# Kernel optimization log

Hardware: AMD Instinct MI355X
Metric: run time of the kernel (lower is better)

## Reference

```python
import jax, jax.numpy as jnp
from jax import lax
import numpy as np

KSIZE = 3        # matching kernel size
RATE = 2         # downsample rate; raw kernel = 2*RATE = 4
FUSE_K = 3       # fusion (diagonal-sum) kernel size
SOFTMAX_SCALE = 10.0
EPS = 1e-4


def extract_patches(x, k, s, pad):
    """im2col: x [B,C,H,W] -> patches [B, L, C, k, k], L = oH*oW (row-major),
    matching torch.nn.Unfold ordering after the view/permute in the source."""
    B, C, H, W = x.shape
    xp = jnp.pad(x, ((0, 0), (0, 0), (pad, pad), (pad, pad)))
    Hp, Wp = H + 2 * pad, W + 2 * pad
    oH = (Hp - k) // s + 1
    oW = (Wp - k) // s + 1
    cols = []
    for i in range(k):
        for j in range(k):
            cols.append(xp[:, :, i:i + (oH - 1) * s + 1:s, j:j + (oW - 1) * s + 1:s])
    p = jnp.stack(cols, axis=0).reshape(k, k, B, C, oH, oW)
    return p.transpose(2, 4, 5, 3, 0, 1).reshape(B, oH * oW, C, k, k)


def fuse_diag(y, k):
    """conv2d with identity (eye(k)) kernel, 'same' padding == sum of diagonal shifts."""
    r = k // 2
    n0, n1 = y.shape
    yp = jnp.pad(y, r)
    return sum(yp[r + d:r + d + n0, r + d:r + d + n1] for d in range(-r, r + 1))


def _per_sample(xi, wi, raw_wi, mi):
    # xi: [C,Hs,Ws] downsampled foreground; wi: [L,C,3,3] bg patches;
    # raw_wi: [L,C,4,4] raw bg patches; mi: [L] patch validity mask
    C, Hs, Ws = xi.shape
    L = wi.shape[0]
    # L2-normalize each background patch (EPS added per-element inside the sum, as in source)
    wi_norm = jnp.sqrt(jnp.sum(wi * wi + EPS, axis=(1, 2, 3), keepdims=True))
    wn = (wi / wi_norm).reshape(L, -1)                      # [L, C*9]
    # correlation scores: conv2d(xi, wi_normed, pad=1) expressed as a GEMM over im2col patches
    fp = extract_patches(xi[None], KSIZE, 1, KSIZE // 2)[0].reshape(L, -1)  # [L_f, C*9]
    yi = wn @ fp.T                                          # [L_b, L_f]
    # fusion trick: identity-kernel conv along both diagonal orientations
    yi = fuse_diag(yi, FUSE_K)
    yi = yi.reshape(Hs, Ws, Hs, Ws).transpose(1, 0, 3, 2).reshape(L, L)
    yi = fuse_diag(yi, FUSE_K)
    yi = yi.reshape(Ws, Hs, Ws, Hs).transpose(1, 0, 3, 2)
    yi = yi.reshape(L, Hs, Ws)
    m = mi[:, None, None]
    yi = jax.nn.softmax(yi * m * SOFTMAX_SCALE, axis=0) * m  # softmax over bg-patch axis
    # transposed conv reconstruction with raw 4x4 patches, stride=RATE, padding=1
    k = 2 * RATE
    w_t = jnp.flip(raw_wi, (2, 3)).transpose(1, 0, 2, 3)     # [C, L, 4, 4] OIHW
    out = lax.conv_general_dilated(
        yi[None], w_t, window_strides=(1, 1),
        padding=[(k - 1 - 1, k - 1 - 1)] * 2, lhs_dilation=(RATE, RATE),
        dimension_numbers=('NCHW', 'OIHW', 'NCHW'))[0] / 4.0  # [C, H, W]
    return out


def setup_inputs() -> dict:
    key = jax.random.key(0)
    k1, k2 = jax.random.split(key)
    B, C, H, W = 4, 128, 96, 96
    b = jax.random.normal(k1, (B, C, H, W), jnp.float32)
    f = jax.random.normal(k2, (B, C, H, W), jnp.float32)
    mask = jnp.ones((B, 1, H, W), jnp.float32)
    return {"b": b, "f": f, "mask": mask}


def reference(b, f, mask):
    B, C, H, W = b.shape
    k_raw = 2 * RATE
    # raw patches from full-res background: k=4, stride=2, pad=1 (get_pad 'valid')
    raw_w = extract_patches(b, k_raw, RATE, 1)               # [B, L, C, 4, 4]
    # nearest downsample by RATE (F.interpolate nearest, scale 1/rate)
    fs = f[:, :, ::RATE, ::RATE]
    bs = b[:, :, ::RATE, ::RATE]
    Hs, Ws = fs.shape[2], fs.shape[3]
    w = extract_patches(bs, KSIZE, 1, KSIZE // 2)            # [B, L, C, 3, 3]
    ms = mask.shape[3] // Ws
    m_small = mask[:, :, ::ms, ::ms]                         # [B, 1, Hs, Ws]
    m = extract_patches(m_small, KSIZE, 1, KSIZE // 2)       # [B, L, 1, 3, 3]
    mm = (jnp.mean(m, axis=(2, 3, 4)) == 1.0).astype(jnp.float32)  # [B, L]
    y = jax.vmap(_per_sample)(fs, w, raw_w, mm)              # [B, C, H, W]
    return y
```

## Files before the change

kernel.cpp:

```cpp
#include <hip/hip_runtime.h>
#include <hip/hip_bf16.h>
#include <math.h>

#define NS   4
#define CH   128
#define HW   96
#define GS   48
#define LL   2304
#define CKN  2048
#define SCALE 10.0f
#define EPSSUM 0.1152f
#define PCH2 32
#define NCH2 72

#define S_IN  ((size_t)CH * HW * HW)
#define S_MK  ((size_t)HW * HW)
#define S_BS  ((size_t)CH * LL)
#define S_PM  ((size_t)NCH2 * LL)
#define S_BUF ((size_t)LL * LL)
#define S_W2  ((size_t)CKN * LL)
#define S_AT  ((size_t)LL * LL)

typedef __attribute__((ext_vector_type(8))) short short8;
typedef __attribute__((ext_vector_type(4))) float float4v;

#define GLDS16(gptr, lptr) \
    __builtin_amdgcn_global_load_lds((const __attribute__((address_space(1))) void*)(gptr), \
        (__attribute__((address_space(3))) void*)(lptr), 16, 0, 0)

__device__ __forceinline__ float4 ld4(const float* p) { return *reinterpret_cast<const float4*>(p); }


__global__ __launch_bounds__(256) void k_stage(const float* __restrict__ b, const float* __restrict__ f,
                                               float* __restrict__ bs_c, float* __restrict__ fs_c) {
    int s = blockIdx.z;
    b += s * S_IN; f += s * S_IN; bs_c += s * S_BS; fs_c += s * S_BS;
    int c  = blockIdx.y;
    int rs = blockIdx.x * 256 + threadIdx.x;
    int r = rs / GS, ss = rs % GS;
    int src = c * HW * HW + (2 * r) * HW + 2 * ss;
    bs_c[c * LL + rs] = b[src];
    fs_c[c * LL + rs] = f[src];
}

__global__ __launch_bounds__(256) void k_ssq(const float* __restrict__ bs_c, float* __restrict__ ssq) {
    int s = blockIdx.z;
    bs_c += s * S_BS; ssq += (size_t)s * LL;
    int rs = blockIdx.x * 256 + threadIdx.x;
    int c0 = blockIdx.y * 32;
    float acc = 0.f;
    for (int c = c0; c < c0 + 32; ++c) { float v = bs_c[c * LL + rs]; acc += v * v; }
    atomicAdd(&ssq[rs], acc);
}

__global__ __launch_bounds__(256) void k_norm_mm(const float* __restrict__ ssq, const float* __restrict__ mk,
                                                 float* __restrict__ invn, float* __restrict__ mmv) {
    int sI = blockIdx.z;
    ssq += (size_t)sI * LL; mk += sI * S_MK; invn += (size_t)sI * LL; mmv += (size_t)sI * LL;
    int p = blockIdx.x * 256 + threadIdx.x;
    int ph = p / GS, pw = p % GS;
    float acc = EPSSUM;
    float msum = 0.f;
    for (int di = -1; di <= 1; ++di)
        for (int dj = -1; dj <= 1; ++dj) {
            int r = ph + di, s = pw + dj;
            if (r >= 0 && r < GS && s >= 0 && s < GS) {
                acc  += ssq[r * GS + s];
                msum += mk[(2 * r) * HW + 2 * s];
            }
        }
    invn[p] = 1.0f / sqrtf(acc);
    mmv[p]  = (msum / 9.0f == 1.0f) ? 1.0f : 0.0f;
}

__global__ __launch_bounds__(256) void k_w2T(const float* __restrict__ b, __hip_bfloat16* __restrict__ W2T) {
    int sI = blockIdx.z;
    b += sI * S_IN; W2T += sI * S_W2;
    int ck = blockIdx.y;
    int p  = blockIdx.x * 256 + threadIdx.x;
    int c = ck >> 4, dy = (ck >> 2) & 3, dx = ck & 3;
    int ph = p / GS, pw = p % GS;
    int r = 2 * ph + dy - 1, s = 2 * pw + dx - 1;
    float v = 0.f;
    if (r >= 0 && r < HW && s >= 0 && s < HW) v = b[c * HW * HW + r * HW + s];
    W2T[(size_t)ck * LL + p] = __float2bfloat16(v);
}

__global__ __launch_bounds__(256) void k_split_T(const float* __restrict__ bs_c, const float* __restrict__ fs_c,
                                                 float* __restrict__ bufB) {
    __shared__ float tile[32][33];
    int z = blockIdx.z;
    int s = z >> 1, sel = z & 1;
    const float* X = (sel ? fs_c : bs_c) + s * S_BS;
    __hip_bfloat16* base = (__hip_bfloat16*)(bufB + s * S_BUF);
    __hip_bfloat16* hi = base + (size_t)sel * 2 * LL * CH;
    __hip_bfloat16* lo = hi + (size_t)LL * CH;
    int r0 = blockIdx.x * 32, c0 = blockIdx.y * 32;
    int tx = threadIdx.x & 31, ty = threadIdx.x >> 5;
#pragma unroll
    for (int j = 0; j < 4; ++j)
        tile[ty + 8 * j][tx] = X[(size_t)(c0 + ty + 8 * j) * LL + r0 + tx];
    __syncthreads();
#pragma unroll
    for (int j = 0; j < 4; ++j) {
        int rl = ty + 8 * j, cl = tx;
        float v = tile[cl][rl];
        __hip_bfloat16 h = __float2bfloat16(v);
        float resid = v - __bfloat162float(h);
        hi[(size_t)(r0 + rl) * CH + c0 + cl] = h;
        lo[(size_t)(r0 + rl) * CH + c0 + cl] = __float2bfloat16(resid);
    }
}

__global__ __launch_bounds__(256) void gemm1_mfma(const float* __restrict__ bufB, float* __restrict__ bufA) {
    __shared__ __hip_bfloat16 sAh[128 * 32];
    __shared__ __hip_bfloat16 sAl[128 * 32];
    __shared__ __hip_bfloat16 sBh[128 * 32];
    __shared__ __hip_bfloat16 sBl[128 * 32];
    int sI = blockIdx.z;
    const __hip_bfloat16* base = (const __hip_bfloat16*)(bufB + sI * S_BUF);
    const __hip_bfloat16* Ahi = base;
    const __hip_bfloat16* Alo = Ahi + (size_t)LL * CH;
    const __hip_bfloat16* Bhi = Alo + (size_t)LL * CH;
    const __hip_bfloat16* Blo = Bhi + (size_t)LL * CH;
    float* C = bufA + sI * S_BUF;

    int t = threadIdx.x, lane = t & 63, w = t >> 6;
    int wr = w >> 1, wc = w & 1;
    int m0 = blockIdx.y * 128, n0 = blockIdx.x * 128;

    float4v acc[4][4];
#pragma unroll
    for (int i = 0; i < 4; ++i)
#pragma unroll
        for (int j = 0; j < 4; ++j) acc[i][j] = (float4v){0.f, 0.f, 0.f, 0.f};

    for (int k0 = 0; k0 < 128; k0 += 32) {
#pragma unroll
        for (int it = 0; it < 2; ++it) {
            int chunk = it * 256 + w * 64 + lane;
            int row = chunk >> 2, ps = chunk & 3;
            int pd = ps ^ (row & 3);
            size_t ga = (size_t)(m0 + row) * 128 + k0 + pd * 8;
            size_t gb = (size_t)(n0 + row) * 128 + k0 + pd * 8;
            GLDS16(Ahi + ga, (char*)sAh + (size_t)chunk * 16);
            GLDS16(Alo + ga, (char*)sAl + (size_t)chunk * 16);
            GLDS16(Bhi + gb, (char*)sBh + (size_t)chunk * 16);
            GLDS16(Blo + gb, (char*)sBl + (size_t)chunk * 16);
        }
        __syncthreads();

        int lrow = lane & 15, part = lane >> 4;
        int sw = part ^ (lrow & 3);
        short8 ah[4], al[4], bh[4], bl[4];
#pragma unroll
        for (int i = 0; i < 4; ++i) {
            int slot = (wr * 64 + i * 16 + lrow) * 4 + sw;
            ah[i] = *reinterpret_cast<const short8*>(sAh + (size_t)slot * 8);
            al[i] = *reinterpret_cast<const short8*>(sAl + (size_t)slot * 8);
        }
#pragma unroll
        for (int j = 0; j < 4; ++j) {
            int slot = (wc * 64 + j * 16 + lrow) * 4 + sw;
            bh[j] = *reinterpret_cast<const short8*>(sBh + (size_t)slot * 8);
            bl[j] = *reinterpret_cast<const short8*>(sBl + (size_t)slot * 8);
        }
#pragma unroll
        for (int i = 0; i < 4; ++i)
#pragma unroll
            for (int j = 0; j < 4; ++j) {
                acc[i][j] = __builtin_amdgcn_mfma_f32_16x16x32_bf16(ah[i], bh[j], acc[i][j], 0, 0, 0);
                acc[i][j] = __builtin_amdgcn_mfma_f32_16x16x32_bf16(ah[i], bl[j], acc[i][j], 0, 0, 0);
                acc[i][j] = __builtin_amdgcn_mfma_f32_16x16x32_bf16(al[i], bh[j], acc[i][j], 0, 0, 0);
            }
        __syncthreads();
    }

    int col = lane & 15, rbase = (lane >> 4) * 4;
#pragma unroll
    for (int i = 0; i < 4; ++i)
#pragma unroll
        for (int j = 0; j < 4; ++j)
#pragma unroll
            for (int r = 0; r < 4; ++r) {
                int m = m0 + wr * 64 + i * 16 + rbase + r;
                int n = n0 + wc * 64 + j * 16 + col;
                C[(size_t)m * LL + n] = acc[i][j][r];
            }
}

__global__ __launch_bounds__(256) void gemm2_mfma(const __hip_bfloat16* __restrict__ W2T_,
                                                  const __hip_bfloat16* __restrict__ attnT_,
                                                  float* __restrict__ bufB) {
    __shared__ __hip_bfloat16 As[128 * 32];
    __shared__ __hip_bfloat16 Bs[128 * 32];
    int sI = blockIdx.z;
    const __hip_bfloat16* A = W2T_ + sI * S_W2;
    const __hip_bfloat16* B = attnT_ + sI * S_AT;
    __hip_bfloat16* C = (__hip_bfloat16*)(bufB + sI * S_BUF);

    int t = threadIdx.x;
    int lane = t & 63, w = t >> 6;
    int wr = w >> 1, wc = w & 1;
    int m0 = blockIdx.y * 128, n0 = blockIdx.x * 128;

    float4v acc[4][4];
#pragma unroll
    for (int i = 0; i < 4; ++i)
#pragma unroll
        for (int j = 0; j < 4; ++j) acc[i][j] = (float4v){0.f, 0.f, 0.f, 0.f};

    for (int k0 = 0; k0 < LL; k0 += 32) {
#pragma unroll
        for (int it = 0; it < 2; ++it) {
            int chunk = it * 256 + w * 64 + lane;
            int row = chunk >> 2, ps = chunk & 3;
            int pd = ps ^ (row & 3);
            const __hip_bfloat16* ga = A + (size_t)(m0 + row) * LL + k0 + pd * 8;
            const __hip_bfloat16* gb = B + (size_t)(n0 + row) * LL + k0 + pd * 8;
            GLDS16(ga, (char*)As + (size_t)chunk * 16);
            GLDS16(gb, (char*)Bs + (size_t)chunk * 16);
        }
        __syncthreads();

        int lrow = lane & 15, part = lane >> 4;
        int sw = part ^ (lrow & 3);
        short8 afrag[4], bfrag[4];
#pragma unroll
        for (int i = 0; i < 4; ++i) {
            int slot = (wr * 64 + i * 16 + lrow) * 4 + sw;
            afrag[i] = *reinterpret_cast<const short8*>(As + (size_t)slot * 8);
        }
#pragma unroll
        for (int j = 0; j < 4; ++j) {
            int slot = (wc * 64 + j * 16 + lrow) * 4 + sw;
            bfrag[j] = *reinterpret_cast<const short8*>(Bs + (size_t)slot * 8);
        }
#pragma unroll
        for (int i = 0; i < 4; ++i)
#pragma unroll
            for (int j = 0; j < 4; ++j)
                acc[i][j] = __builtin_amdgcn_mfma_f32_16x16x32_bf16(afrag[i], bfrag[j], acc[i][j], 0, 0, 0);
        __syncthreads();
    }

    int col = lane & 15, rbase = (lane >> 4) * 4;
#pragma unroll
    for (int i = 0; i < 4; ++i)
#pragma unroll
        for (int j = 0; j < 4; ++j)
#pragma unroll
            for (int r = 0; r < 4; ++r) {
                int m = m0 + wr * 64 + i * 16 + rbase + r;
                int n = n0 + wc * 64 + j * 16 + col;
                C[(size_t)m * LL + n] = __float2bfloat16(acc[i][j][r]);
            }
}

__global__ __launch_bounds__(192) void k_corr_v4(const float* __restrict__ bufA, const float* __restrict__ invn,
                                                 float* __restrict__ bufB) {
    int sI = blockIdx.z;
    const float* D = bufA + sI * S_BUF;
    float* yi = bufB + sI * S_BUF;
    invn += (size_t)sI * LL;

    int p  = blockIdx.y;
    int qi = blockIdx.x * 192 + threadIdx.x;
    int q4 = qi * 4;
    int qh = q4 / GS, qw0 = q4 % GS;
    int ph = p / GS, pw = p % GS;

    float4 acc = {0.f, 0.f, 0.f, 0.f};
#pragma unroll
    for (int di = -1; di <= 1; ++di) {
        int rp = ph + di, tq = qh + di;
        if (rp < 0 || rp >= GS || tq < 0 || tq >= GS) continue;
        int r0 = rp * GS + pw;
        int c0 = tq * GS + qw0;
        {
            float4 Cc = ld4(D + (size_t)r0 * LL + c0);
            acc.x += Cc.x; acc.y += Cc.y; acc.z += Cc.z; acc.w += Cc.w;
        }
        if (pw > 0) {
            const float* rowm = D + (size_t)(r0 - 1) * LL;
            float4 L  = ld4(rowm + (qw0 > 0 ? c0 - 4 : c0));
            float4 Cm = ld4(rowm + c0);
            acc.x += (qw0 > 0 ? L.w : 0.f);
            acc.y += Cm.x; acc.z += Cm.y; acc.w += Cm.z;
        }
        if (pw < GS - 1) {
            const float* rowp = D + (size_t)(r0 + 1) * LL;
            float4 Cp = ld4(rowp + c0);
            float4 R  = ld4(rowp + (qw0 < GS - 4 ? c0 + 4 : c0));
            acc.x += Cp.y; acc.y += Cp.z; acc.z += Cp.w;
            acc.w += (qw0 < GS - 4 ? R.x : 0.f);
        }
    }
    float inv = invn[p];
    float4 outv = {inv * acc.x, inv * acc.y, inv * acc.z, inv * acc.w};
    *reinterpret_cast<float4*>(yi + (size_t)p * LL + q4) = outv;
}

__device__ __forceinline__ int gmap(int x) { int hi = x / GS; int lo = x - hi * GS; return lo * GS + hi; }

__global__ __launch_bounds__(256) void k_fuse2_sm(const float* __restrict__ bufB, const float* __restrict__ mmv,
                                                  float* __restrict__ bufA,
                                                  float* __restrict__ pmax, float* __restrict__ psum) {
    int sI = blockIdx.z;
    const float* yi = bufB + sI * S_BUF;
    float* S2 = bufA + sI * S_BUF;
    mmv += (size_t)sI * LL; pmax += sI * S_PM; psum += sI * S_PM;
    int q = blockIdx.x * 256 + threadIdx.x;
    int qh = q / GS, qw = q % GS;
    int b0 = qw * GS + qh;
    int p0 = blockIdx.y * PCH2;
    float mx = -1e30f, sm = 0.f;
    for (int i = 0; i < PCH2; ++i) {
        int p = p0 + i;
        int ph = p / GS, pw = p % GS;
        int a0 = pw * GS + ph;
        float s = 0.f;
#pragma unroll
        for (int e = -1; e <= 1; ++e) {
            int ae = a0 + e, be = b0 + e;
            if (ae < 0 || ae >= LL || be < 0 || be >= LL) continue;
            int A = gmap(ae), B = gmap(be);
#pragma unroll
            for (int d = -1; d <= 1; ++d) {
                int Ad = A + d, Bd = B + d;
                if (Ad >= 0 && Ad < LL && Bd >= 0 && Bd < LL)
                    s += yi[(size_t)Ad * LL + Bd];
            }
        }
        S2[(size_t)p * LL + q] = s;
        float lg = (mmv[p] != 0.f) ? SCALE * s : 0.f;
        float nm = fmaxf(mx, lg);
        sm = sm * __expf(mx - nm) + __expf(lg - nm);
        mx = nm;
    }
    pmax[blockIdx.y * LL + q] = mx;
    psum[blockIdx.y * LL + q] = sm;
}

__global__ __launch_bounds__(256) void k_sm2(const float* __restrict__ pmax, const float* __restrict__ psum,
                                             float* __restrict__ Mq, float* __restrict__ Dq) {
    __shared__ float red[4][64];
    int sI = blockIdx.z;
    pmax += sI * S_PM; psum += sI * S_PM; Mq += (size_t)sI * LL; Dq += (size_t)sI * LL;
    int t = threadIdx.x;
    int ql = t & 63, g = t >> 6;
    int q = blockIdx.x * 64 + ql;
    float mx = -1e30f;
    for (int ch = g * 18; ch < g * 18 + 18; ++ch) mx = fmaxf(mx, pmax[(size_t)ch * LL + q]);
    red[g][ql] = mx;
    __syncthreads();
    float mall = fmaxf(fmaxf(red[0][ql], red[1][ql]), fmaxf(red[2][ql], red[3][ql]));
    float sm = 0.f;
    for (int ch = g * 18; ch < g * 18 + 18; ++ch)
        sm += psum[(size_t)ch * LL + q] * __expf(pmax[(size_t)ch * LL + q] - mall);
    __syncthreads();
    red[g][ql] = sm;
    __syncthreads();
    if (g == 0) {
        Mq[q] = mall;
        Dq[q] = (red[0][ql] + red[1][ql]) + (red[2][ql] + red[3][ql]);
    }
}

__global__ __launch_bounds__(256) void k_sm3T(const float* __restrict__ S2buf, const float* __restrict__ mmv,
                                              const float* __restrict__ Mq, const float* __restrict__ Dq,
                                              __hip_bfloat16* __restrict__ attnT) {
    __shared__ float tile[32][33];
    int sI = blockIdx.z;
    const float* S2 = S2buf + sI * S_BUF;
    mmv += (size_t)sI * LL; Mq += (size_t)sI * LL; Dq += (size_t)sI * LL; attnT += sI * S_AT;
    int tx = threadIdx.x & 31, ty = threadIdx.x >> 5;
    int p0 = blockIdx.y * 32, q0 = blockIdx.x * 32;
    int q = q0 + tx;
    float mq = Mq[q], dq = Dq[q];
#pragma unroll
    for (int j = 0; j < 4; ++j) {
        int p = p0 + ty + 8 * j;
        float v = S2[(size_t)p * LL + q];
        float attn = (mmv[p] != 0.f) ? __expf(SCALE * v - mq) / dq : 0.f;
        tile[ty + 8 * j][tx] = attn;
    }
    __syncthreads();
#pragma unroll
    for (int j = 0; j < 4; ++j) {
        int qq = q0 + ty + 8 * j;
        attnT[(size_t)qq * LL + p0 + tx] = __float2bfloat16(tile[tx][ty + 8 * j]);
    }
}

__global__ __launch_bounds__(256) void k_out(const float* __restrict__ bufB, float* __restrict__ out) {
    int sI = blockIdx.z;
    const __hip_bfloat16* Z = (const __hip_bfloat16*)(bufB + sI * S_BUF);
    out += sI * S_IN;
    int c  = blockIdx.y;
    int yx = blockIdx.x * 256 + threadIdx.x;
    int y = yx / HW, x = yx % HW;
    int u = y >> 1, a = y & 1, v = x >> 1, w = x & 1;
    int qh1 = u + a - 1, qh2 = u + a, qw1 = v + w - 1, qw2 = v + w;
    int cb = c * 16;
    float s = 0.f;
    if (qh1 >= 0) {
        if (qw1 >= 0)  s += __bfloat162float(Z[(size_t)(cb + (3 - a) * 4 + (3 - w)) * LL + qh1 * GS + qw1]);
        if (qw2 < GS)  s += __bfloat162float(Z[(size_t)(cb + (3 - a) * 4 + (1 - w)) * LL + qh1 * GS + qw2]);
    }
    if (qh2 < GS) {
        if (qw1 >= 0)  s += __bfloat162float(Z[(size_t)(cb + (1 - a) * 4 + (3 - w)) * LL + qh2 * GS + qw1]);
        if (qw2 < GS)  s += __bfloat162float(Z[(size_t)(cb + (1 - a) * 4 + (1 - w)) * LL + qh2 * GS + qw2]);
    }
    out[(size_t)c * HW * HW + yx] = 0.25f * s;
}


extern "C" void kernel_launch(void* const* d_in, const int* in_sizes, int n_in,
                              void* d_out, int out_size, void* d_ws, size_t ws_size,
                              hipStream_t stream) {
    const float* b_all = (const float*)d_in[0];
    const float* f_all = (const float*)d_in[1];
    const float* m_all = (const float*)d_in[2];
    float* out = (float*)d_out;
    float* ws  = (float*)d_ws;

    const size_t perF = 2 * S_BS + 5 * (size_t)LL + 2 * S_PM + 2 * S_BUF + S_W2 / 2 + S_AT / 2;
    const size_t perB = perF * sizeof(float);
    int nb = (ws_size >= NS * perB) ? NS : ((ws_size >= 2 * perB) ? 2 : 1);

    size_t off = 0;
    float* bs_c = ws + off; off += nb * S_BS;
    float* fs_c = ws + off; off += nb * S_BS;
    float* ssq  = ws + off; off += nb * (size_t)LL;
    float* invn = ws + off; off += nb * (size_t)LL;
    float* mmv  = ws + off; off += nb * (size_t)LL;
    float* Mq   = ws + off; off += nb * (size_t)LL;
    float* Dq   = ws + off; off += nb * (size_t)LL;
    float* pmax = ws + off; off += nb * S_PM;
    float* psum = ws + off; off += nb * S_PM;
    float* bufA = ws + off; off += nb * S_BUF;
    float* bufB = ws + off; off += nb * S_BUF;
    __hip_bfloat16* W2T   = (__hip_bfloat16*)(ws + off); off += nb * S_W2 / 2;
    __hip_bfloat16* attnT = (__hip_bfloat16*)(ws + off); off += nb * S_AT / 2;

    for (int s0 = 0; s0 < NS; s0 += nb) {
        const float* b  = b_all + s0 * S_IN;
        const float* f  = f_all + s0 * S_IN;
        const float* mk = m_all + s0 * S_MK;
        float* outp = out + s0 * S_IN;

        hipMemsetAsync(ssq, 0, nb * LL * sizeof(float), stream);
        k_stage    <<<dim3(9, CH, nb), 256, 0, stream>>>(b, f, bs_c, fs_c);
        k_ssq      <<<dim3(9, 4, nb), 256, 0, stream>>>(bs_c, ssq);
        k_norm_mm  <<<dim3(9, 1, nb), 256, 0, stream>>>(ssq, mk, invn, mmv);
        k_w2T      <<<dim3(9, CKN, nb), 256, 0, stream>>>(b, W2T);
        k_split_T  <<<dim3(72, 4, 2 * nb), 256, 0, stream>>>(bs_c, fs_c, bufB);

        gemm1_mfma <<<dim3(18, 18, nb), 256, 0, stream>>>(bufB, bufA);
        k_corr_v4  <<<dim3(3, LL, nb), 192, 0, stream>>>(bufA, invn, bufB);
        k_fuse2_sm <<<dim3(9, NCH2, nb), 256, 0, stream>>>(bufB, mmv, bufA, pmax, psum);

        k_sm2      <<<dim3(36, 1, nb), 256, 0, stream>>>(pmax, psum, Mq, Dq);
        k_sm3T     <<<dim3(72, 72, nb), 256, 0, stream>>>(bufA, mmv, Mq, Dq, attnT);

        gemm2_mfma <<<dim3(LL / 128, CKN / 128, nb), 256, 0, stream>>>(W2T, attnT, bufB);
        k_out      <<<dim3(36, CH, nb), 256, 0, stream>>>(bufB, outp);
    }
}
```

Baseline: 587.4 us.

## Split diagonal fusion into separable passes with LDS ring buffer and vectorized second pass

Restructures the two diagonal-sum fusion stages. The first kernel now computes the normalized correlation rows and applies the first diagonal fusion in a rolling three-row shared-memory buffer, so each row is produced once. The second kernel reads the already-fused rows with float4 loads, producing four outputs per thread with per-column online softmax statistics, replacing the nine scattered loads per element. Buffer roles for gemm2 and the output kernel are swapped to fit the new dataflow. In exchange, the first kernel uses large blocks with shared memory and serialized barriers per row, and the second pass falls back to gathered loads at the boundaries.

```diff
diff --git a/kernel.cpp b/kernel.cpp
--- a/kernel.cpp
+++ b/kernel.cpp
@@ -12,6 +12,7 @@
 #define EPSSUM 0.1152f
 #define PCH2 32
 #define NCH2 72
+#define TPF  16
 
 #define S_IN  ((size_t)CH * HW * HW)
 #define S_MK  ((size_t)HW * HW)
@@ -191,13 +192,13 @@
 
 __global__ __launch_bounds__(256) void gemm2_mfma(const __hip_bfloat16* __restrict__ W2T_,
                                                   const __hip_bfloat16* __restrict__ attnT_,
-                                                  float* __restrict__ bufB) {
+                                                  float* __restrict__ bufA) {
     __shared__ __hip_bfloat16 As[128 * 32];
     __shared__ __hip_bfloat16 Bs[128 * 32];
     int sI = blockIdx.z;
     const __hip_bfloat16* A = W2T_ + sI * S_W2;
     const __hip_bfloat16* B = attnT_ + sI * S_AT;
-    __hip_bfloat16* C = (__hip_bfloat16*)(bufB + sI * S_BUF);
+    __hip_bfloat16* C = (__hip_bfloat16*)(bufA + sI * S_BUF);
 
     int t = threadIdx.x;
     int lane = t & 63, w = t >> 6;
@@ -257,89 +258,136 @@
             }
 }
 
-__global__ __launch_bounds__(192) void k_corr_v4(const float* __restrict__ bufA, const float* __restrict__ invn,
-                                                 float* __restrict__ bufB) {
+__global__ __launch_bounds__(576) void k_corr_fuse1(const float* __restrict__ bufA, const float* __restrict__ invn,
+                                                    float* __restrict__ bufB) {
+    __shared__ float L[3][LL];
     int sI = blockIdx.z;
     const float* D = bufA + sI * S_BUF;
-    float* yi = bufB + sI * S_BUF;
+    float* S1 = bufB + sI * S_BUF;
     invn += (size_t)sI * LL;
-
-    int p  = blockIdx.y;
+    int a0 = blockIdx.x * TPF;
+    int t = threadIdx.x;
+    int q4 = t * 4;
+    int qh = q4 / GS, qw0 = q4 % GS;
+
+    auto produce = [&](int p) {
+        int slot = ((p % 3) + 3) % 3;
+        float4 o = {0.f, 0.f, 0.f, 0.f};
+        if (p >= 0 && p < LL) {
+            int ph = p / GS, pw = p % GS;
+            float4 acc = {0.f, 0.f, 0.f, 0.f};
+#pragma unroll
+            for (int di = -1; di <= 1; ++di) {
+                int rp = ph + di, tq = qh + di;
+                if (rp < 0 || rp >= GS || tq < 0 || tq >= GS) continue;
+                int r0 = rp * GS + pw;
+                int c0 = tq * GS + qw0;
+                {
+                    float4 Cc = ld4(D + (size_t)r0 * LL + c0);
+                    acc.x += Cc.x; acc.y += Cc.y; acc.z += Cc.z; acc.w += Cc.w;
+                }
+                if (pw > 0) {
+                    const float* rowm = D + (size_t)(r0 - 1) * LL;
+                    float4 Lq = ld4(rowm + (qw0 > 0 ? c0 - 4 : c0));
+                    float4 Cm = ld4(rowm + c0);
+                    acc.x += (qw0 > 0 ? Lq.w : 0.f);
+                    acc.y += Cm.x; acc.z += Cm.y; acc.w += Cm.z;
+                }
+                if (pw < GS - 1) {
+                    const float* rowp = D + (size_t)(r0 + 1) * LL;
+                    float4 Cp = ld4(rowp + c0);
+                    float4 Rq = ld4(rowp + (qw0 < GS - 4 ? c0 + 4 : c0));
+                    acc.x += Cp.y; acc.y += Cp.z; acc.z += Cp.w;
+                    acc.w += (qw0 < GS - 4 ? Rq.x : 0.f);
+                }
+            }
+            float inv = invn[p];
+            o.x = inv * acc.x; o.y = inv * acc.y; o.z = inv * acc.z; o.w = inv * acc.w;
+        }
+        *reinterpret_cast<float4*>(&L[slot][q4]) = o;
+    };
+
+    produce(a0 - 1);
+    produce(a0);
+    __syncthreads();
+    for (int r = a0; r < a0 + TPF; ++r) {
+        produce(r + 1);
+        __syncthreads();
+        int sm1 = ((r - 1) % 3 + 3) % 3, s0 = r % 3, sp1 = (r + 1) % 3;
+        float4 acc = *reinterpret_cast<const float4*>(&L[s0][q4]);
+        {
+            float4 Cm = *reinterpret_cast<const float4*>(&L[sm1][q4]);
+            float lm = (q4 > 0) ? L[sm1][q4 - 1] : 0.f;
+            acc.x += lm; acc.y += Cm.x; acc.z += Cm.y; acc.w += Cm.z;
+        }
+        {
+            float4 Cp = *reinterpret_cast<const float4*>(&L[sp1][q4]);
+            float rp = (q4 + 4 < LL) ? L[sp1][q4 + 4] : 0.f;
+            acc.x += Cp.y; acc.y += Cp.z; acc.z += Cp.w; acc.w += rp;
+        }
+        *reinterpret_cast<float4*>(S1 + (size_t)r * LL + q4) = acc;
+        __syncthreads();
+    }
+}
+
+__device__ __forceinline__ int gmap(int x) { int hi = x / GS; int lo = x - hi * GS; return lo * GS + hi; }
+
+__global__ __launch_bounds__(192) void k_fuse2_sm_v4(const float* __restrict__ bufB, const float* __restrict__ mmv,
+                                                     float* __restrict__ bufA,
+                                                     float* __restrict__ pmax, float* __restrict__ psum) {
+    int sI = blockIdx.z;
+    const float* S1 = bufB + sI * S_BUF;
+    float* S2 = bufA + sI * S_BUF;
+    mmv += (size_t)sI * LL; pmax += sI * S_PM; psum += sI * S_PM;
     int qi = blockIdx.x * 192 + threadIdx.x;
     int q4 = qi * 4;
     int qh = q4 / GS, qw0 = q4 % GS;
-    int ph = p / GS, pw = p % GS;
-
-    float4 acc = {0.f, 0.f, 0.f, 0.f};
-#pragma unroll
-    for (int di = -1; di <= 1; ++di) {
-        int rp = ph + di, tq = qh + di;
-        if (rp < 0 || rp >= GS || tq < 0 || tq >= GS) continue;
-        int r0 = rp * GS + pw;
-        int c0 = tq * GS + qw0;
-        {
-            float4 Cc = ld4(D + (size_t)r0 * LL + c0);
-            acc.x += Cc.x; acc.y += Cc.y; acc.z += Cc.z; acc.w += Cc.w;
-        }
-        if (pw > 0) {
-            const float* rowm = D + (size_t)(r0 - 1) * LL;
-            float4 L  = ld4(rowm + (qw0 > 0 ? c0 - 4 : c0));
-            float4 Cm = ld4(rowm + c0);
-            acc.x += (qw0 > 0 ? L.w : 0.f);
-            acc.y += Cm.x; acc.z += Cm.y; acc.w += Cm.z;
-        }
-        if (pw < GS - 1) {
-            const float* rowp = D + (size_t)(r0 + 1) * LL;
-            float4 Cp = ld4(rowp + c0);
-            float4 R  = ld4(rowp + (qw0 < GS - 4 ? c0 + 4 : c0));
-            acc.x += Cp.y; acc.y += Cp.z; acc.z += Cp.w;
-            acc.w += (qw0 < GS - 4 ? R.x : 0.f);
-        }
-    }
-    float inv = invn[p];
-    float4 outv = {inv * acc.x, inv * acc.y, inv * acc.z, inv * acc.w};
-    *reinterpret_cast<float4*>(yi + (size_t)p * LL + q4) = outv;
-}
-
-__device__ __forceinline__ int gmap(int x) { int hi = x / GS; int lo = x - hi * GS; return lo * GS + hi; }
-
-__global__ __launch_bounds__(256) void k_fuse2_sm(const float* __restrict__ bufB, const float* __restrict__ mmv,
-                                                  float* __restrict__ bufA,
-                                                  float* __restrict__ pmax, float* __restrict__ psum) {
-    int sI = blockIdx.z;
-    const float* yi = bufB + sI * S_BUF;
-    float* S2 = bufA + sI * S_BUF;
-    mmv += (size_t)sI * LL; pmax += sI * S_PM; psum += sI * S_PM;
-    int q = blockIdx.x * 256 + threadIdx.x;
-    int qh = q / GS, qw = q % GS;
-    int b0 = qw * GS + qh;
     int p0 = blockIdx.y * PCH2;
-    float mx = -1e30f, sm = 0.f;
+    float mxa[4], sma[4];
+#pragma unroll
+    for (int j = 0; j < 4; ++j) { mxa[j] = -1e30f; sma[j] = 0.f; }
+
     for (int i = 0; i < PCH2; ++i) {
         int p = p0 + i;
         int ph = p / GS, pw = p % GS;
         int a0 = pw * GS + ph;
-        float s = 0.f;
+        float sarr[4] = {0.f, 0.f, 0.f, 0.f};
 #pragma unroll
         for (int e = -1; e <= 1; ++e) {
-            int ae = a0 + e, be = b0 + e;
-            if (ae < 0 || ae >= LL || be < 0 || be >= LL) continue;
-            int A = gmap(ae), B = gmap(be);
-#pragma unroll
-            for (int d = -1; d <= 1; ++d) {
-                int Ad = A + d, Bd = B + d;
-                if (Ad >= 0 && Ad < LL && Bd >= 0 && Bd < LL)
-                    s += yi[(size_t)Ad * LL + Bd];
+            int ae = a0 + e;
+            if (ae < 0 || ae >= LL) continue;
+            int Ar = gmap(ae);
+            const float* Rw = S1 + (size_t)Ar * LL;
+            int qe = qh + e;
+            if (qe >= 0 && qe < GS) {
+                float4 v = ld4(Rw + q4 + 48 * e);
+                sarr[0] += v.x; sarr[1] += v.y; sarr[2] += v.z; sarr[3] += v.w;
+            } else {
+#pragma unroll
+                for (int j = 0; j < 4; ++j) {
+                    int be = (qw0 + j) * GS + qh + e;
+                    if (be >= 0 && be < LL) {
+                        int bh = be / GS, bw = be % GS;
+                        sarr[j] += Rw[bw * GS + bh];
+                    }
+                }
             }
         }
-        S2[(size_t)p * LL + q] = s;
-        float lg = (mmv[p] != 0.f) ? SCALE * s : 0.f;
-        float nm = fmaxf(mx, lg);
-        sm = sm * __expf(mx - nm) + __expf(lg - nm);
-        mx = nm;
-    }
-    pmax[blockIdx.y * LL + q] = mx;
-    psum[blockIdx.y * LL + q] = sm;
+        float4 sv = {sarr[0], sarr[1], sarr[2], sarr[3]};
+        *reinterpret_cast<float4*>(S2 + (size_t)p * LL + q4) = sv;
+        float mv = mmv[p];
+#pragma unroll
+        for (int j = 0; j < 4; ++j) {
+            float lg = (mv != 0.f) ? SCALE * sarr[j] : 0.f;
+            float nm = fmaxf(mxa[j], lg);
+            sma[j] = sma[j] * __expf(mxa[j] - nm) + __expf(lg - nm);
+            mxa[j] = nm;
+        }
+    }
+    float4 mo = {mxa[0], mxa[1], mxa[2], mxa[3]};
+    float4 so = {sma[0], sma[1], sma[2], sma[3]};
+    *reinterpret_cast<float4*>(pmax + blockIdx.y * LL + q4) = mo;
+    *reinterpret_cast<float4*>(psum + blockIdx.y * LL + q4) = so;
 }
 
 __global__ __launch_bounds__(256) void k_sm2(const float* __restrict__ pmax, const float* __restrict__ psum,
@@ -393,9 +441,9 @@
     }
 }
 
-__global__ __launch_bounds__(256) void k_out(const float* __restrict__ bufB, float* __restrict__ out) {
-    int sI = blockIdx.z;
-    const __hip_bfloat16* Z = (const __hip_bfloat16*)(bufB + sI * S_BUF);
+__global__ __launch_bounds__(256) void k_out(const float* __restrict__ bufA, float* __restrict__ out) {
+    int sI = blockIdx.z;
+    const __hip_bfloat16* Z = (const __hip_bfloat16*)(bufA + sI * S_BUF);
     out += sI * S_IN;
     int c  = blockIdx.y;
     int yx = blockIdx.x * 256 + threadIdx.x;
@@ -457,14 +505,14 @@
         k_w2T      <<<dim3(9, CKN, nb), 256, 0, stream>>>(b, W2T);
         k_split_T  <<<dim3(72, 4, 2 * nb), 256, 0, stream>>>(bs_c, fs_c, bufB);
 
-        gemm1_mfma <<<dim3(18, 18, nb), 256, 0, stream>>>(bufB, bufA);
-        k_corr_v4  <<<dim3(3, LL, nb), 192, 0, stream>>>(bufA, invn, bufB);
-        k_fuse2_sm <<<dim3(9, NCH2, nb), 256, 0, stream>>>(bufB, mmv, bufA, pmax, psum);
+        gemm1_mfma   <<<dim3(18, 18, nb), 256, 0, stream>>>(bufB, bufA);
+        k_corr_fuse1 <<<dim3(LL / TPF, 1, nb), 576, 0, stream>>>(bufA, invn, bufB);
+        k_fuse2_sm_v4<<<dim3(3, NCH2, nb), 192, 0, stream>>>(bufB, mmv, bufA, pmax, psum);
 
         k_sm2      <<<dim3(36, 1, nb), 256, 0, stream>>>(pmax, psum, Mq, Dq);
         k_sm3T     <<<dim3(72, 72, nb), 256, 0, stream>>>(bufA, mmv, Mq, Dq, attnT);
 
-        gemm2_mfma <<<dim3(LL / 128, CKN / 128, nb), 256, 0, stream>>>(W2T, attnT, bufB);
-        k_out      <<<dim3(36, CH, nb), 256, 0, stream>>>(bufB, outp);
-    }
-}
+        gemm2_mfma <<<dim3(LL / 128, CKN / 128, nb), 256, 0, stream>>>(W2T, attnT, bufA);
+        k_out      <<<dim3(36, CH, nb), 256, 0, stream>>>(bufA, outp);
+    }
+}
```

New measurement: 550.9 us. -6.2%, faster.
